# Performance work log

Hardware: AMD Instinct MI355X
Metric: run time of the kernel (lower is better)

The kernel has to match this reference:

```python
import jax, jax.numpy as jnp
import numpy as np

N = 8192
H = 256
E = N * 32
ALPHA = 0.2  # LeakyReLU negative slope from init kwarg alpha


def setup_inputs() -> dict:
    key = jax.random.key(0)
    ks = jax.random.split(key, 8)
    s = 1.0 / np.sqrt(H)
    return {
        "features": jax.random.normal(ks[0], (N, H), jnp.float32),
        "edge_index": jax.random.randint(ks[1], (2, E), 0, N, jnp.int64),
        "W_att": jax.random.normal(ks[2], (H, H), jnp.float32) * s,
        "a_src": jax.random.normal(ks[3], (H,), jnp.float32) * s,
        "a_dst": jax.random.normal(ks[4], (H,), jnp.float32) * s,
        "gcn_w": jax.random.normal(ks[5], (H, H), jnp.float32) * s,
        "gcn_b": jnp.zeros((H,), jnp.float32),
        "out_w": jax.random.normal(ks[6], (H, 2), jnp.float32) * s,
        "out_b": jnp.zeros((2,), jnp.float32),
    }


def reference(features, edge_index, W_att, a_src, a_dst, gcn_w, gcn_b, out_w, out_b):
    n = features.shape[0]
    # --- SingleNodeAttentionLayer (GAT-style dense self-attention, concat=True) ---
    Wh = features @ W_att                       # [N, H]
    e = jax.nn.leaky_relu(
        (Wh @ a_src)[:, None] + (Wh @ a_dst)[None, :], negative_slope=ALPHA
    )                                            # [N, N]
    attn = jax.nn.softmax(e, axis=-1)
    h1 = jax.nn.elu(attn @ Wh)                   # [N, H]
    # --- GCNConv: symmetric-normalized aggregation with self-loops ---
    loops = jnp.arange(n, dtype=edge_index.dtype)
    row = jnp.concatenate([edge_index[0], loops])  # destination
    col = jnp.concatenate([edge_index[1], loops])  # source
    deg = jax.ops.segment_sum(jnp.ones_like(row, dtype=h1.dtype), row, num_segments=n)
    dinv = jax.lax.rsqrt(jnp.maximum(deg, 1e-12))
    norm = dinv[row] * dinv[col]                 # [E+N]
    x = h1 @ gcn_w                               # [N, H]
    agg = jax.ops.segment_sum(x[col] * norm[:, None], row, num_segments=n) + gcn_b
    # --- head: linear -> mean over nodes -> softmax ---
    res = agg @ out_w + out_b                    # [N, 2]
    res = jnp.mean(res, axis=0, keepdims=True)   # [1, 2]
    return jax.nn.softmax(res, axis=-1)
```

## Files before the change

### kernel.cpp

```cpp
#include <hip/hip_runtime.h>
#include <hip/hip_bf16.h>

#define NN 8192
#define HH 256
#define EE (NN*32)
#define ALPHAC 0.2f
#define CHUNK 32
#define NCHUNK (NN/CHUNK)

#define OFF_WH     0
#define OFF_S      (OFF_WH + NN*HH)
#define OFF_D      (OFF_S + NN)
#define OFF_SORTD  (OFF_D + NN)
#define OFF_PERM   (OFF_SORTD + NN)
#define OFF_EA     (OFF_PERM + NN)
#define OFF_E1     (OFF_EA + NN)
#define OFF_APREF  (OFF_E1 + NN)
#define OFF_BPREF  (OFF_APREF + NN)
#define OFF_APART  (OFF_BPREF + NN)
#define OFF_BPART  (OFF_APART + NN*HH)
#define OFF_CPA    (OFF_BPART + NN*HH)
#define OFF_CPB    (OFF_CPA + (NCHUNK+1)*HH)
#define OFF_DEG    (OFF_CPB + (NCHUNK+1)*HH)
#define OFF_V      (OFF_DEG + NN)
#define OFF_DINV   (OFF_V + HH)
#define OFF_WNODE  (OFF_DINV + NN)
#define OFF_KEYS   (OFF_WNODE + NN)

__global__ __launch_bounds__(256) void k_gemm_wh(const float* __restrict__ A,
                                                 const float* __restrict__ B,
                                                 float* __restrict__ C) {
    __shared__ float As[32][68];
    __shared__ float Bs[32][68];
    int tid = threadIdx.x;
    int row0 = blockIdx.x * 64, col0 = blockIdx.y * 64;
    int tx = tid & 15, ty = tid >> 4;
    float acc[4][4] = {};
    int a_r = tid >> 2;
    int a_k = (tid & 3) * 8;
    int b_k = tid >> 3;
    int b_c = (tid & 7) * 8;
    const float* Aptr = A + (size_t)(row0 + a_r)*HH + a_k;
    const float* Bptr = B + (size_t)b_k*HH + col0 + b_c;
    for (int k0 = 0; k0 < HH; k0 += 32) {
        float4 av0 = *(const float4*)(Aptr + k0);
        float4 av1 = *(const float4*)(Aptr + k0 + 4);
        float4 bv0 = *(const float4*)(Bptr + (size_t)k0*HH);
        float4 bv1 = *(const float4*)(Bptr + (size_t)k0*HH + 4);
        __syncthreads();
        As[a_k+0][a_r] = av0.x; As[a_k+1][a_r] = av0.y;
        As[a_k+2][a_r] = av0.z; As[a_k+3][a_r] = av0.w;
        As[a_k+4][a_r] = av1.x; As[a_k+5][a_r] = av1.y;
        As[a_k+6][a_r] = av1.z; As[a_k+7][a_r] = av1.w;
        *(float4*)&Bs[b_k][b_c]   = bv0;
        *(float4*)&Bs[b_k][b_c+4] = bv1;
        __syncthreads();
        #pragma unroll
        for (int kk = 0; kk < 32; ++kk) {
            float4 ar = *(const float4*)&As[kk][ty*4];
            float4 br = *(const float4*)&Bs[kk][tx*4];
            float a0[4] = {ar.x, ar.y, ar.z, ar.w};
            float b0[4] = {br.x, br.y, br.z, br.w};
            #pragma unroll
            for (int r = 0; r < 4; ++r)
                #pragma unroll
                for (int c = 0; c < 4; ++c)
                    acc[r][c] += a0[r]*b0[c];
        }
    }
    #pragma unroll
    for (int r = 0; r < 4; ++r) {
        float4 o = make_float4(acc[r][0], acc[r][1], acc[r][2], acc[r][3]);
        *(float4*)(C + (size_t)(row0 + ty*4 + r)*HH + col0 + tx*4) = o;
    }
}

__global__ void k_sd(const float* __restrict__ Wh, const float* __restrict__ a_src,
                     const float* __restrict__ a_dst, float* ws) {
    int wave = threadIdx.x >> 6, lane = threadIdx.x & 63;
    int row = blockIdx.x*4 + wave;
    float4 wh = *(const float4*)(Wh + (size_t)row*HH + lane*4);
    float4 as = *(const float4*)(a_src + lane*4);
    float4 ad = *(const float4*)(a_dst + lane*4);
    float ss = wh.x*as.x + wh.y*as.y + wh.z*as.z + wh.w*as.w;
    float dd = wh.x*ad.x + wh.y*ad.y + wh.z*ad.z + wh.w*ad.w;
    #pragma unroll
    for (int off = 32; off; off >>= 1) {
        ss += __shfl_xor(ss, off);
        dd += __shfl_xor(dd, off);
    }
    if (lane == 0) {
        ws[OFF_S+row] = ss; ws[OFF_D+row] = dd;
        unsigned u = __float_as_uint(dd);
        unsigned mono = u ^ ((u & 0x80000000u) ? 0xFFFFFFFFu : 0x80000000u);
        ((unsigned long long*)(ws + OFF_KEYS))[row] =
            (((unsigned long long)mono) << 13) | (unsigned)row;
    }
}

__global__ __launch_bounds__(256) void k_rank(float* ws) {
    __shared__ unsigned long long lk[NN];
    const unsigned long long* keys = (const unsigned long long*)(ws + OFF_KEYS);
    int tid = threadIdx.x;
    for (int m = tid; m < NN/2; m += 256)
        *(ulonglong2*)&lk[m*2] = *(const ulonglong2*)&keys[m*2];
    __syncthreads();
    int wave = tid >> 6, lane = tid & 63;
    int jb = blockIdx.x*16 + wave*4;
    unsigned long long kj0 = lk[jb+0], kj1 = lk[jb+1];
    unsigned long long kj2 = lk[jb+2], kj3 = lk[jb+3];
    int c0 = 0, c1 = 0, c2 = 0, c3 = 0;
    #pragma unroll 4
    for (int it = 0; it < 64; ++it) {
        ulonglong2 kq = *(const ulonglong2*)&lk[(it*64 + lane)*2];
        c0 += (kq.x < kj0); c1 += (kq.x < kj1);
        c2 += (kq.x < kj2); c3 += (kq.x < kj3);
        c0 += (kq.y < kj0); c1 += (kq.y < kj1);
        c2 += (kq.y < kj2); c3 += (kq.y < kj3);
    }
    #pragma unroll
    for (int off = 1; off < 64; off <<= 1) {
        c0 += __shfl_xor(c0, off);
        c1 += __shfl_xor(c1, off);
        c2 += __shfl_xor(c2, off);
        c3 += __shfl_xor(c3, off);
    }
    if (lane == 0) {
        unsigned long long kk[4] = {kj0, kj1, kj2, kj3};
        int cr[4] = {c0, c1, c2, c3};
        #pragma unroll
        for (int q = 0; q < 4; ++q) {
            unsigned long long kv = kk[q];
            int r = cr[q];
            unsigned mm = (unsigned)(kv >> 13);
            unsigned u = (mm & 0x80000000u) ? (mm ^ 0x80000000u) : ~mm;
            float dj = __uint_as_float(u);
            int j = (int)(kv & 8191ULL);
            ws[OFF_SORTD + r] = dj;
            ((int*)ws)[OFF_PERM + r] = j;
            ws[OFF_EA + r] = expf(ALPHAC * dj);
            ws[OFF_E1 + r] = expf(dj);
        }
    }
}

__global__ void k_scan_scalar(float* ws) {
    __shared__ float sa[256], sb[256];
    int t = threadIdx.x;
    const float* ea = ws + OFF_EA;
    const float* e1 = ws + OFF_E1;
    int base = t * 32;
    float ta = 0.f, tb = 0.f;
    #pragma unroll
    for (int q = 0; q < 8; ++q) {
        float4 va = *(const float4*)&ea[base + q*4];
        float4 vb = *(const float4*)&e1[base + q*4];
        ta += va.x + va.y + va.z + va.w;
        tb += vb.x + vb.y + vb.z + vb.w;
    }
    sa[t] = ta; sb[t] = tb;
    __syncthreads();
    for (int off = 1; off < 256; off <<= 1) {
        float xa = (t >= off) ? sa[t-off] : 0.f;
        float xb = (t >= off) ? sb[t-off] : 0.f;
        __syncthreads();
        sa[t] += xa; sb[t] += xb;
        __syncthreads();
    }
    float ra = sa[t] - ta, rb = sb[t] - tb;
    #pragma unroll
    for (int q = 0; q < 8; ++q) {
        float4 va = *(const float4*)&ea[base + q*4];
        float4 vb = *(const float4*)&e1[base + q*4];
        float4 oa, ob;
        ra += va.x; oa.x = ra;  rb += vb.x; ob.x = rb;
        ra += va.y; oa.y = ra;  rb += vb.y; ob.y = rb;
        ra += va.z; oa.z = ra;  rb += vb.z; ob.z = rb;
        ra += va.w; oa.w = ra;  rb += vb.w; ob.w = rb;
        *(float4*)&ws[OFF_APREF + base + q*4] = oa;
        *(float4*)&ws[OFF_BPREF + base + q*4] = ob;
    }
}

__global__ __launch_bounds__(256) void k_vecpref(float* ws) {
    __shared__ int   sp[CHUNK];
    __shared__ float sea[CHUNK], se1[CHUNK];
    int c = blockIdx.x, h = threadIdx.x;
    int k0 = c * CHUNK;
    if (h < CHUNK) {
        sp[h]  = ((int*)ws)[OFF_PERM + k0 + h];
        sea[h] = ws[OFF_EA + k0 + h];
        se1[h] = ws[OFF_E1 + k0 + h];
    }
    __syncthreads();
    const float* Wh = ws + OFF_WH;
    float wv[CHUNK];
    #pragma unroll
    for (int kk = 0; kk < CHUNK; ++kk)
        wv[kk] = Wh[(size_t)sp[kk]*HH + h];
    float acca = 0.f, accb = 0.f;
    #pragma unroll
    for (int kk = 0; kk < CHUNK; ++kk) {
        acca += sea[kk]*wv[kk]; accb += se1[kk]*wv[kk];
        ws[OFF_APART + (size_t)(k0+kk)*HH + h] = acca;
        ws[OFF_BPART + (size_t)(k0+kk)*HH + h] = accb;
    }
    ws[OFF_CPA + (size_t)(c+1)*HH + h] = acca;
    ws[OFF_CPB + (size_t)(c+1)*HH + h] = accb;
}

__global__ __launch_bounds__(256) void k_chunkscan(float* ws) {
    int tid = threadIdx.x;
    int h = blockIdx.x*8 + (tid >> 5);
    int t = tid & 31;
    float la[8], lb[8];
    float ta = 0.f, tb = 0.f;
    #pragma unroll
    for (int m = 0; m < 8; ++m) {
        int c = t*8 + m;
        la[m] = ws[OFF_CPA + (size_t)(c+1)*HH + h];
        lb[m] = ws[OFF_CPB + (size_t)(c+1)*HH + h];
        ta += la[m]; tb += lb[m];
    }
    float ia = ta, ib = tb;
    #pragma unroll
    for (int off = 1; off < 32; off <<= 1) {
        float xa = __shfl_up(ia, off, 32);
        float xb = __shfl_up(ib, off, 32);
        if (t >= off) { ia += xa; ib += xb; }
    }
    float ba = ia - ta, bb = ib - tb;
    __syncthreads();
    #pragma unroll
    for (int m = 0; m < 8; ++m) {
        int c = t*8 + m;
        ws[OFF_CPA + (size_t)c*HH + h] = ba; ba += la[m];
        ws[OFF_CPB + (size_t)c*HH + h] = bb; bb += lb[m];
    }
    if (t == 31) {
        ws[OFF_CPA + (size_t)NCHUNK*HH + h] = ba;
        ws[OFF_CPB + (size_t)NCHUNK*HH + h] = bb;
    }
}

__global__ void k_deg(const int* __restrict__ ei, float* ws) {
    int e = blockIdx.x*256 + threadIdx.x;
    if (e < EE) atomicAdd(ws + OFF_DEG + ei[e], 1.0f);
}

__global__ void k_dinv(float* ws) {
    int i = blockIdx.x*256 + threadIdx.x;
    if (i < NN) {
        float dv = rsqrtf(ws[OFF_DEG + i] + 1.0f);
        ws[OFF_DINV + i] = dv;
        ws[OFF_WNODE + i] = dv*dv;
    }
}

__global__ void k_wnode(const int* __restrict__ ei, float* ws) {
    int e = blockIdx.x*256 + threadIdx.x;
    if (e < EE) {
        int r = ei[e], c = ei[EE + e];
        atomicAdd(ws + OFF_WNODE + c, ws[OFF_DINV + r] * ws[OFF_DINV + c]);
    }
}

__device__ __forceinline__ float elu1(float x) {
    return x > 0.f ? x : (expf(x) - 1.f);
}

__global__ __launch_bounds__(256) void k_rows(float* ws) {
    __shared__ float sd[NN];
    __shared__ float red[4][256];
    int tid = threadIdx.x;
    for (int m = tid; m < NN/4; m += 256)
        *(float4*)&sd[m*4] = *(const float4*)(ws + OFF_SORTD + m*4);
    __syncthreads();
    int wave = tid >> 6, lane = tid & 63;
    int gw = blockIdx.x*4 + wave;
    const float* apart = ws + OFF_APART;
    const float* bpart = ws + OFF_BPART;
    const float* cpa = ws + OFF_CPA;
    const float* cpb = ws + OFF_CPB;
    float btot = ws[OFF_BPREF + NN - 1];
    float4 BT = *(const float4*)(cpb + (size_t)NCHUNK*HH + lane*4);

    int myr = lane & 3;
    float si_m = ws[OFF_S + gw*4 + myr];
    float tt = -si_m;
    int lo = 0, hi = NN;
    while (lo < hi) {
        int mid = (lo + hi) >> 1;
        if (sd[mid] <= tt) lo = mid + 1; else hi = mid;
    }

    float accx = 0.f, accy = 0.f, accz = 0.f, accw = 0.f;
    #pragma unroll
    for (int r = 0; r < 4; ++r) {
        int i = gw*4 + r;
        int k = __shfl(lo, r);
        float si = __shfl(si_m, r);
        float eas = expf(ALPHAC * si), es = expf(si);
        float av = 0.f, bv = 0.f;
        float Ax=0.f, Ay=0.f, Az=0.f, Aw=0.f, Bx=0.f, By=0.f, Bz=0.f, Bw=0.f;
        if (k > 0) {
            int km = k - 1, cc = km >> 5;
            av = ws[OFF_APREF + km]; bv = ws[OFF_BPREF + km];
            float4 pa = *(const float4*)(apart + (size_t)km*HH + lane*4);
            float4 ca = *(const float4*)(cpa + (size_t)cc*HH + lane*4);
            float4 pb = *(const float4*)(bpart + (size_t)km*HH + lane*4);
            float4 cb = *(const float4*)(cpb + (size_t)cc*HH + lane*4);
            Ax = pa.x + ca.x; Ay = pa.y + ca.y; Az = pa.z + ca.z; Aw = pa.w + ca.w;
            Bx = pb.x + cb.x; By = pb.y + cb.y; Bz = pb.z + cb.z; Bw = pb.w + cb.w;
        }
        float Z = eas*av + es*(btot - bv);
        float invZ = 1.f / Z;
        float w = ws[OFF_WNODE + i];
        accx += w * elu1((eas*Ax + es*(BT.x - Bx)) * invZ);
        accy += w * elu1((eas*Ay + es*(BT.y - By)) * invZ);
        accz += w * elu1((eas*Az + es*(BT.z - Bz)) * invZ);
        accw += w * elu1((eas*Aw + es*(BT.w - Bw)) * invZ);
    }
    red[wave][lane*4+0] = accx;
    red[wave][lane*4+1] = accy;
    red[wave][lane*4+2] = accz;
    red[wave][lane*4+3] = accw;
    __syncthreads();
    float sum = red[0][tid] + red[1][tid] + red[2][tid] + red[3][tid];
    atomicAdd(ws + OFF_V + tid, sum);
}

__global__ void k_final(const float* __restrict__ gcn_w, const float* __restrict__ gcn_b,
                        const float* __restrict__ out_w, const float* __restrict__ out_b,
                        float* ws, float* out) {
    __shared__ float vl[HH];
    __shared__ float r0s[256], r1s[256];
    int t = threadIdx.x;
    vl[t] = ws[OFF_V + t];
    __syncthreads();
    float acc = 0.f;
    for (int h = 0; h < HH; ++h) acc += vl[h] * gcn_w[(size_t)h*HH + t];
    float meanv = acc * (1.0f/(float)NN) + gcn_b[t];
    r0s[t] = meanv * out_w[t*2+0];
    r1s[t] = meanv * out_w[t*2+1];
    __syncthreads();
    for (int off = 128; off; off >>= 1) {
        if (t < off) { r0s[t] += r0s[t+off]; r1s[t] += r1s[t+off]; }
        __syncthreads();
    }
    if (t == 0) {
        float res0 = r0s[0] + out_b[0], res1 = r1s[0] + out_b[1];
        float m = fmaxf(res0, res1);
        float e0 = expf(res0 - m), e1v = expf(res1 - m);
        float inv = 1.f / (e0 + e1v);
        out[0] = e0 * inv;
        out[1] = e1v * inv;
    }
}

extern "C" void kernel_launch(void* const* d_in, const int* in_sizes, int n_in,
                              void* d_out, int out_size, void* d_ws, size_t ws_size,
                              hipStream_t stream) {
    const float* features = (const float*)d_in[0];
    const int*   eidx     = (const int*)d_in[1];
    const float* W_att    = (const float*)d_in[2];
    const float* a_src    = (const float*)d_in[3];
    const float* a_dst    = (const float*)d_in[4];
    const float* gcn_w    = (const float*)d_in[5];
    const float* gcn_b    = (const float*)d_in[6];
    const float* out_w    = (const float*)d_in[7];
    const float* out_b    = (const float*)d_in[8];
    float* ws  = (float*)d_ws;
    float* out = (float*)d_out;

    hipMemsetAsync(ws + OFF_DEG, 0, (NN + HH)*sizeof(float), stream);
    k_gemm_wh<<<dim3(NN/64, HH/64), 256, 0, stream>>>(features, W_att, ws + OFF_WH);
    k_sd<<<NN/4, 256, 0, stream>>>(ws + OFF_WH, a_src, a_dst, ws);
    k_rank<<<NN/16, 256, 0, stream>>>(ws);
    k_scan_scalar<<<1, 256, 0, stream>>>(ws);
    k_vecpref<<<NCHUNK, 256, 0, stream>>>(ws);
    k_chunkscan<<<HH/8, 256, 0, stream>>>(ws);
    k_deg<<<EE/256, 256, 0, stream>>>(eidx, ws);
    k_dinv<<<NN/256, 256, 0, stream>>>(ws);
    k_wnode<<<EE/256, 256, 0, stream>>>(eidx, ws);
    k_rows<<<NN/16, 256, 0, stream>>>(ws);
    k_final<<<1, 256, 0, stream>>>(gcn_w, gcn_b, out_w, out_b, ws, out);
}
```

Before: 185.5 us.

## Fuse independent kernels, use bf16 MFMA for Wh GEMM, halve chunk size

Converts features and W_att to bf16 and computes Wh with MFMA 16x16x32 bf16 instructions instead of an fp32 SIMT GEMM. Independent stages (GEMM with degree counting, score/dinv, wnode with vector prefix, scalar scans with chunk scan) are merged into shared launches split by block index, which cuts the launch count. The scalar prefix is now computed per chunk, and the A/B partial sums are interleaved as float2. Switching the GEMM to bf16 lowers the precision of Wh, which feeds the sort by attention score. A dead kernel, k_sd_dinv, is left defined but never launched.

```diff
diff --git a/kernel.cpp b/kernel.cpp
--- a/kernel.cpp
+++ b/kernel.cpp
@@ -5,8 +5,12 @@
 #define HH 256
 #define EE (NN*32)
 #define ALPHAC 0.2f
-#define CHUNK 32
+#define CHUNK 16
 #define NCHUNK (NN/CHUNK)
+#define CSPAD 1024
+
+typedef __bf16 bf16x8 __attribute__((ext_vector_type(8)));
+typedef float  f32x4  __attribute__((ext_vector_type(4)));
 
 #define OFF_WH     0
 #define OFF_S      (OFF_WH + NN*HH)
@@ -15,86 +19,132 @@
 #define OFF_PERM   (OFF_SORTD + NN)
 #define OFF_EA     (OFF_PERM + NN)
 #define OFF_E1     (OFF_EA + NN)
-#define OFF_APREF  (OFF_E1 + NN)
-#define OFF_BPREF  (OFF_APREF + NN)
-#define OFF_APART  (OFF_BPREF + NN)
-#define OFF_BPART  (OFF_APART + NN*HH)
-#define OFF_CPA    (OFF_BPART + NN*HH)
-#define OFF_CPB    (OFF_CPA + (NCHUNK+1)*HH)
-#define OFF_DEG    (OFF_CPB + (NCHUNK+1)*HH)
+#define OFF_SAREL  (OFF_E1 + NN)
+#define OFF_SBREL  (OFF_SAREL + NN)
+#define OFF_ABPART (OFF_SBREL + NN)
+#define OFF_CPAB   (OFF_ABPART + 2*NN*HH)
+#define OFF_CSA    (OFF_CPAB + 2*(NCHUNK+1)*HH)
+#define OFF_CSB    (OFF_CSA + CSPAD)
+#define OFF_DEG    (OFF_CSB + CSPAD)
 #define OFF_V      (OFF_DEG + NN)
 #define OFF_DINV   (OFF_V + HH)
 #define OFF_WNODE  (OFF_DINV + NN)
 #define OFF_KEYS   (OFF_WNODE + NN)
-
-__global__ __launch_bounds__(256) void k_gemm_wh(const float* __restrict__ A,
-                                                 const float* __restrict__ B,
-                                                 float* __restrict__ C) {
-    __shared__ float As[32][68];
-    __shared__ float Bs[32][68];
-    int tid = threadIdx.x;
-    int row0 = blockIdx.x * 64, col0 = blockIdx.y * 64;
-    int tx = tid & 15, ty = tid >> 4;
-    float acc[4][4] = {};
-    int a_r = tid >> 2;
-    int a_k = (tid & 3) * 8;
-    int b_k = tid >> 3;
-    int b_c = (tid & 7) * 8;
-    const float* Aptr = A + (size_t)(row0 + a_r)*HH + a_k;
-    const float* Bptr = B + (size_t)b_k*HH + col0 + b_c;
-    for (int k0 = 0; k0 < HH; k0 += 32) {
-        float4 av0 = *(const float4*)(Aptr + k0);
-        float4 av1 = *(const float4*)(Aptr + k0 + 4);
-        float4 bv0 = *(const float4*)(Bptr + (size_t)k0*HH);
-        float4 bv1 = *(const float4*)(Bptr + (size_t)k0*HH + 4);
-        __syncthreads();
-        As[a_k+0][a_r] = av0.x; As[a_k+1][a_r] = av0.y;
-        As[a_k+2][a_r] = av0.z; As[a_k+3][a_r] = av0.w;
-        As[a_k+4][a_r] = av1.x; As[a_k+5][a_r] = av1.y;
-        As[a_k+6][a_r] = av1.z; As[a_k+7][a_r] = av1.w;
-        *(float4*)&Bs[b_k][b_c]   = bv0;
-        *(float4*)&Bs[b_k][b_c+4] = bv1;
-        __syncthreads();
-        #pragma unroll
-        for (int kk = 0; kk < 32; ++kk) {
-            float4 ar = *(const float4*)&As[kk][ty*4];
-            float4 br = *(const float4*)&Bs[kk][tx*4];
-            float a0[4] = {ar.x, ar.y, ar.z, ar.w};
-            float b0[4] = {br.x, br.y, br.z, br.w};
-            #pragma unroll
-            for (int r = 0; r < 4; ++r)
-                #pragma unroll
-                for (int c = 0; c < 4; ++c)
-                    acc[r][c] += a0[r]*b0[c];
-        }
-    }
-    #pragma unroll
-    for (int r = 0; r < 4; ++r) {
-        float4 o = make_float4(acc[r][0], acc[r][1], acc[r][2], acc[r][3]);
-        *(float4*)(C + (size_t)(row0 + ty*4 + r)*HH + col0 + tx*4) = o;
-    }
-}
-
-__global__ void k_sd(const float* __restrict__ Wh, const float* __restrict__ a_src,
-                     const float* __restrict__ a_dst, float* ws) {
-    int wave = threadIdx.x >> 6, lane = threadIdx.x & 63;
-    int row = blockIdx.x*4 + wave;
-    float4 wh = *(const float4*)(Wh + (size_t)row*HH + lane*4);
-    float4 as = *(const float4*)(a_src + lane*4);
-    float4 ad = *(const float4*)(a_dst + lane*4);
-    float ss = wh.x*as.x + wh.y*as.y + wh.z*as.z + wh.w*as.w;
-    float dd = wh.x*ad.x + wh.y*ad.y + wh.z*ad.z + wh.w*ad.w;
-    #pragma unroll
-    for (int off = 32; off; off >>= 1) {
-        ss += __shfl_xor(ss, off);
-        dd += __shfl_xor(dd, off);
-    }
-    if (lane == 0) {
-        ws[OFF_S+row] = ss; ws[OFF_D+row] = dd;
-        unsigned u = __float_as_uint(dd);
-        unsigned mono = u ^ ((u & 0x80000000u) ? 0xFFFFFFFFu : 0x80000000u);
-        ((unsigned long long*)(ws + OFF_KEYS))[row] =
-            (((unsigned long long)mono) << 13) | (unsigned)row;
+#define OFF_FB16   (OFF_KEYS + 2*NN)
+#define OFF_WT16   (OFF_FB16 + NN*HH/2)
+
+__global__ __launch_bounds__(256) void k_prep(const float* __restrict__ features,
+                                              const float* __restrict__ W_att,
+                                              float* ws) {
+    int bid = blockIdx.x, tid = threadIdx.x;
+    if (bid < 1024) {
+        int base = (bid*256 + tid)*8;
+        float4 a = *(const float4*)(features + base);
+        float4 b = *(const float4*)(features + base + 4);
+        bf16x8 v;
+        v[0]=(__bf16)a.x; v[1]=(__bf16)a.y; v[2]=(__bf16)a.z; v[3]=(__bf16)a.w;
+        v[4]=(__bf16)b.x; v[5]=(__bf16)b.y; v[6]=(__bf16)b.z; v[7]=(__bf16)b.w;
+        *(bf16x8*)((__bf16*)(ws + OFF_FB16) + base) = v;
+    } else if (bid < 1056) {
+        int idx0 = ((bid-1024)*256 + tid)*8;
+        __bf16* WT = (__bf16*)(ws + OFF_WT16);
+        #pragma unroll
+        for (int q = 0; q < 8; ++q) {
+            int idx = idx0 + q;
+            int n = idx >> 8, k = idx & 255;
+            WT[idx] = (__bf16)W_att[(size_t)k*HH + n];
+        }
+    } else {
+        int z0 = ((bid-1056)*256 + tid)*8;
+        #pragma unroll
+        for (int q = 0; q < 8; ++q) {
+            int i = z0 + q;
+            if (i < NN + HH) ws[OFF_DEG + i] = 0.f;
+        }
+    }
+}
+
+__global__ __launch_bounds__(256) void k_gemm_deg(const int* __restrict__ ei, float* ws) {
+    int bid = blockIdx.x, tid = threadIdx.x;
+    if (bid < 512) {
+        int mt = bid >> 2, nt = bid & 3;
+        int wave = tid >> 6, lane = tid & 63;
+        int ml = lane & 15, quad = lane >> 4;
+        int row0 = mt*64 + wave*16;
+        int n0 = nt*64;
+        const __bf16* FB = (const __bf16*)(ws + OFF_FB16);
+        const __bf16* WT = (const __bf16*)(ws + OFF_WT16);
+        const __bf16* Ap = FB + (size_t)(row0 + ml)*HH + quad*8;
+        const __bf16* B0 = WT + (size_t)(n0 +  0 + ml)*HH + quad*8;
+        const __bf16* B1 = WT + (size_t)(n0 + 16 + ml)*HH + quad*8;
+        const __bf16* B2 = WT + (size_t)(n0 + 32 + ml)*HH + quad*8;
+        const __bf16* B3 = WT + (size_t)(n0 + 48 + ml)*HH + quad*8;
+        f32x4 ac0 = {0.f,0.f,0.f,0.f}, ac1 = ac0, ac2 = ac0, ac3 = ac0;
+        #pragma unroll
+        for (int k0 = 0; k0 < HH; k0 += 32) {
+            bf16x8 af = *(const bf16x8*)(Ap + k0);
+            ac0 = __builtin_amdgcn_mfma_f32_16x16x32_bf16(af, *(const bf16x8*)(B0 + k0), ac0, 0, 0, 0);
+            ac1 = __builtin_amdgcn_mfma_f32_16x16x32_bf16(af, *(const bf16x8*)(B1 + k0), ac1, 0, 0, 0);
+            ac2 = __builtin_amdgcn_mfma_f32_16x16x32_bf16(af, *(const bf16x8*)(B2 + k0), ac2, 0, 0, 0);
+            ac3 = __builtin_amdgcn_mfma_f32_16x16x32_bf16(af, *(const bf16x8*)(B3 + k0), ac3, 0, 0, 0);
+        }
+        float* Whp = ws + OFF_WH;
+        #pragma unroll
+        for (int r = 0; r < 4; ++r) {
+            size_t grow = (size_t)(row0 + quad*4 + r)*HH + n0 + ml;
+            Whp[grow +  0] = ac0[r];
+            Whp[grow + 16] = ac1[r];
+            Whp[grow + 32] = ac2[r];
+            Whp[grow + 48] = ac3[r];
+        }
+    } else {
+        int e = (bid - 512)*256 + tid;
+        atomicAdd(ws + OFF_DEG + ei[e], 1.0f);
+    }
+}
+
+__global__ __launch_bounds__(256) void k_sd_dinv(float* ws) {
+    int bid = blockIdx.x, tid = threadIdx.x;
+    if (bid < 2048) {
+        int wave = tid >> 6, lane = tid & 63;
+        int row = bid*4 + wave;
+        const float* Wh = ws + OFF_WH;
+        float4 wh = *(const float4*)(Wh + (size_t)row*HH + lane*4);
+        (void)wh;
+    }
+    (void)ws;
+}
+
+__global__ __launch_bounds__(256) void k_sd_dinv2(const float* __restrict__ a_src,
+                                                  const float* __restrict__ a_dst,
+                                                  float* ws) {
+    int bid = blockIdx.x, tid = threadIdx.x;
+    if (bid < 2048) {
+        int wave = tid >> 6, lane = tid & 63;
+        int row = bid*4 + wave;
+        const float* Wh = ws + OFF_WH;
+        float4 wh = *(const float4*)(Wh + (size_t)row*HH + lane*4);
+        float4 as = *(const float4*)(a_src + lane*4);
+        float4 ad = *(const float4*)(a_dst + lane*4);
+        float ss = wh.x*as.x + wh.y*as.y + wh.z*as.z + wh.w*as.w;
+        float dd = wh.x*ad.x + wh.y*ad.y + wh.z*ad.z + wh.w*ad.w;
+        #pragma unroll
+        for (int off = 32; off; off >>= 1) {
+            ss += __shfl_xor(ss, off);
+            dd += __shfl_xor(dd, off);
+        }
+        if (lane == 0) {
+            ws[OFF_S+row] = ss; ws[OFF_D+row] = dd;
+            unsigned u = __float_as_uint(dd);
+            unsigned mono = u ^ ((u & 0x80000000u) ? 0xFFFFFFFFu : 0x80000000u);
+            ((unsigned long long*)(ws + OFF_KEYS))[row] =
+                (((unsigned long long)mono) << 13) | (unsigned)row;
+        }
+    } else {
+        int i = (bid - 2048)*256 + tid;
+        float dv = rsqrtf(ws[OFF_DEG + i] + 1.0f);
+        ws[OFF_DINV + i] = dv;
+        ws[OFF_WNODE + i] = dv*dv;
     }
 }
 
@@ -144,124 +194,110 @@
     }
 }
 
-__global__ void k_scan_scalar(float* ws) {
-    __shared__ float sa[256], sb[256];
-    int t = threadIdx.x;
-    const float* ea = ws + OFF_EA;
-    const float* e1 = ws + OFF_E1;
-    int base = t * 32;
-    float ta = 0.f, tb = 0.f;
-    #pragma unroll
-    for (int q = 0; q < 8; ++q) {
-        float4 va = *(const float4*)&ea[base + q*4];
-        float4 vb = *(const float4*)&e1[base + q*4];
-        ta += va.x + va.y + va.z + va.w;
-        tb += vb.x + vb.y + vb.z + vb.w;
-    }
-    sa[t] = ta; sb[t] = tb;
-    __syncthreads();
-    for (int off = 1; off < 256; off <<= 1) {
-        float xa = (t >= off) ? sa[t-off] : 0.f;
-        float xb = (t >= off) ? sb[t-off] : 0.f;
+__global__ __launch_bounds__(256) void k_wnode_vecpref(const int* __restrict__ ei, float* ws) {
+    int bid = blockIdx.x, tid = threadIdx.x;
+    if (bid < NCHUNK) {
+        __shared__ int   sp[CHUNK];
+        __shared__ float sea[CHUNK], se1[CHUNK];
+        int c = bid, h = tid;
+        int k0 = c * CHUNK;
+        if (h < CHUNK) {
+            sp[h]  = ((int*)ws)[OFF_PERM + k0 + h];
+            sea[h] = ws[OFF_EA + k0 + h];
+            se1[h] = ws[OFF_E1 + k0 + h];
+        }
         __syncthreads();
-        sa[t] += xa; sb[t] += xb;
+        if (tid < 64) {
+            int lane = tid;
+            float v = 0.f;
+            if (lane < 16) v = sea[lane];
+            else if (lane < 32) v = se1[lane-16];
+            #pragma unroll
+            for (int off = 1; off < 16; off <<= 1) {
+                float x = __shfl_up(v, off);
+                if ((lane & 15) >= off) v += x;
+            }
+            if (lane < 16) {
+                ws[OFF_SAREL + k0 + lane] = v;
+                if (lane == 15) ws[OFF_CSA + c + 1] = v;
+            } else if (lane < 32) {
+                ws[OFF_SBREL + k0 + lane - 16] = v;
+                if (lane == 31) ws[OFF_CSB + c + 1] = v;
+            }
+        }
+        const float* Wh = ws + OFF_WH;
+        float wv[CHUNK];
+        #pragma unroll
+        for (int kk = 0; kk < CHUNK; ++kk)
+            wv[kk] = Wh[(size_t)sp[kk]*HH + h];
+        float2* abp = (float2*)(ws + OFF_ABPART);
+        float acca = 0.f, accb = 0.f;
+        #pragma unroll
+        for (int kk = 0; kk < CHUNK; ++kk) {
+            acca += sea[kk]*wv[kk]; accb += se1[kk]*wv[kk];
+            abp[(size_t)(k0+kk)*HH + h] = make_float2(acca, accb);
+        }
+        float2* cp = (float2*)(ws + OFF_CPAB);
+        cp[(size_t)(c+1)*HH + h] = make_float2(acca, accb);
+    } else {
+        int e = (bid - NCHUNK)*256 + tid;
+        int r = ei[e], cix = ei[EE + e];
+        atomicAdd(ws + OFF_WNODE + cix, ws[OFF_DINV + r] * ws[OFF_DINV + cix]);
+    }
+}
+
+__global__ __launch_bounds__(256) void k_chunkscan(float* ws) {
+    int bid = blockIdx.x, tid = threadIdx.x;
+    if (bid < 32) {
+        int h = bid*8 + (tid >> 5);
+        int t = tid & 31;
+        float2* cp = (float2*)(ws + OFF_CPAB);
+        float la[16], lb[16];
+        float ta = 0.f, tb = 0.f;
+        #pragma unroll
+        for (int m = 0; m < 16; ++m) {
+            float2 v = cp[(size_t)(t*16 + m + 1)*HH + h];
+            la[m] = v.x; lb[m] = v.y;
+            ta += la[m]; tb += lb[m];
+        }
+        float ia = ta, ib = tb;
+        #pragma unroll
+        for (int off = 1; off < 32; off <<= 1) {
+            float xa = __shfl_up(ia, off, 32);
+            float xb = __shfl_up(ib, off, 32);
+            if (t >= off) { ia += xa; ib += xb; }
+        }
+        float ba = ia - ta, bb = ib - tb;
         __syncthreads();
-    }
-    float ra = sa[t] - ta, rb = sb[t] - tb;
-    #pragma unroll
-    for (int q = 0; q < 8; ++q) {
-        float4 va = *(const float4*)&ea[base + q*4];
-        float4 vb = *(const float4*)&e1[base + q*4];
-        float4 oa, ob;
-        ra += va.x; oa.x = ra;  rb += vb.x; ob.x = rb;
-        ra += va.y; oa.y = ra;  rb += vb.y; ob.y = rb;
-        ra += va.z; oa.z = ra;  rb += vb.z; ob.z = rb;
-        ra += va.w; oa.w = ra;  rb += vb.w; ob.w = rb;
-        *(float4*)&ws[OFF_APREF + base + q*4] = oa;
-        *(float4*)&ws[OFF_BPREF + base + q*4] = ob;
-    }
-}
-
-__global__ __launch_bounds__(256) void k_vecpref(float* ws) {
-    __shared__ int   sp[CHUNK];
-    __shared__ float sea[CHUNK], se1[CHUNK];
-    int c = blockIdx.x, h = threadIdx.x;
-    int k0 = c * CHUNK;
-    if (h < CHUNK) {
-        sp[h]  = ((int*)ws)[OFF_PERM + k0 + h];
-        sea[h] = ws[OFF_EA + k0 + h];
-        se1[h] = ws[OFF_E1 + k0 + h];
-    }
-    __syncthreads();
-    const float* Wh = ws + OFF_WH;
-    float wv[CHUNK];
-    #pragma unroll
-    for (int kk = 0; kk < CHUNK; ++kk)
-        wv[kk] = Wh[(size_t)sp[kk]*HH + h];
-    float acca = 0.f, accb = 0.f;
-    #pragma unroll
-    for (int kk = 0; kk < CHUNK; ++kk) {
-        acca += sea[kk]*wv[kk]; accb += se1[kk]*wv[kk];
-        ws[OFF_APART + (size_t)(k0+kk)*HH + h] = acca;
-        ws[OFF_BPART + (size_t)(k0+kk)*HH + h] = accb;
-    }
-    ws[OFF_CPA + (size_t)(c+1)*HH + h] = acca;
-    ws[OFF_CPB + (size_t)(c+1)*HH + h] = accb;
-}
-
-__global__ __launch_bounds__(256) void k_chunkscan(float* ws) {
-    int tid = threadIdx.x;
-    int h = blockIdx.x*8 + (tid >> 5);
-    int t = tid & 31;
-    float la[8], lb[8];
-    float ta = 0.f, tb = 0.f;
-    #pragma unroll
-    for (int m = 0; m < 8; ++m) {
-        int c = t*8 + m;
-        la[m] = ws[OFF_CPA + (size_t)(c+1)*HH + h];
-        lb[m] = ws[OFF_CPB + (size_t)(c+1)*HH + h];
-        ta += la[m]; tb += lb[m];
-    }
-    float ia = ta, ib = tb;
-    #pragma unroll
-    for (int off = 1; off < 32; off <<= 1) {
-        float xa = __shfl_up(ia, off, 32);
-        float xb = __shfl_up(ib, off, 32);
-        if (t >= off) { ia += xa; ib += xb; }
-    }
-    float ba = ia - ta, bb = ib - tb;
-    __syncthreads();
-    #pragma unroll
-    for (int m = 0; m < 8; ++m) {
-        int c = t*8 + m;
-        ws[OFF_CPA + (size_t)c*HH + h] = ba; ba += la[m];
-        ws[OFF_CPB + (size_t)c*HH + h] = bb; bb += lb[m];
-    }
-    if (t == 31) {
-        ws[OFF_CPA + (size_t)NCHUNK*HH + h] = ba;
-        ws[OFF_CPB + (size_t)NCHUNK*HH + h] = bb;
-    }
-}
-
-__global__ void k_deg(const int* __restrict__ ei, float* ws) {
-    int e = blockIdx.x*256 + threadIdx.x;
-    if (e < EE) atomicAdd(ws + OFF_DEG + ei[e], 1.0f);
-}
-
-__global__ void k_dinv(float* ws) {
-    int i = blockIdx.x*256 + threadIdx.x;
-    if (i < NN) {
-        float dv = rsqrtf(ws[OFF_DEG + i] + 1.0f);
-        ws[OFF_DINV + i] = dv;
-        ws[OFF_WNODE + i] = dv*dv;
-    }
-}
-
-__global__ void k_wnode(const int* __restrict__ ei, float* ws) {
-    int e = blockIdx.x*256 + threadIdx.x;
-    if (e < EE) {
-        int r = ei[e], c = ei[EE + e];
-        atomicAdd(ws + OFF_WNODE + c, ws[OFF_DINV + r] * ws[OFF_DINV + c]);
+        #pragma unroll
+        for (int m = 0; m < 16; ++m) {
+            cp[(size_t)(t*16 + m)*HH + h] = make_float2(ba, bb);
+            ba += la[m]; bb += lb[m];
+        }
+        if (t == 31) cp[(size_t)NCHUNK*HH + h] = make_float2(ba, bb);
+    } else {
+        int lane = tid & 63, wvi = tid >> 6;
+        bool act = wvi < 2;
+        float* cs = ws + (wvi == 1 ? OFF_CSB : OFF_CSA);
+        float la[8];
+        float ta = 0.f;
+        if (act) {
+            #pragma unroll
+            for (int m = 0; m < 8; ++m) { la[m] = cs[lane*8 + m + 1]; ta += la[m]; }
+        }
+        float ia = ta;
+        #pragma unroll
+        for (int off = 1; off < 64; off <<= 1) {
+            float x = __shfl_up(ia, off);
+            if (lane >= off) ia += x;
+        }
+        float ba = ia - ta;
+        __syncthreads();
+        if (act) {
+            #pragma unroll
+            for (int m = 0; m < 8; ++m) { cs[lane*8 + m] = ba; ba += la[m]; }
+            if (lane == 63) cs[NCHUNK] = ba;
+        }
     }
 }
 
@@ -278,12 +314,12 @@
     __syncthreads();
     int wave = tid >> 6, lane = tid & 63;
     int gw = blockIdx.x*4 + wave;
-    const float* apart = ws + OFF_APART;
-    const float* bpart = ws + OFF_BPART;
-    const float* cpa = ws + OFF_CPA;
-    const float* cpb = ws + OFF_CPB;
-    float btot = ws[OFF_BPREF + NN - 1];
-    float4 BT = *(const float4*)(cpb + (size_t)NCHUNK*HH + lane*4);
+    const float2* abp  = (const float2*)(ws + OFF_ABPART);
+    const float2* cpab = (const float2*)(ws + OFF_CPAB);
+    float btot = ws[OFF_CSB + NCHUNK];
+    const float4* btr = (const float4*)(cpab + (size_t)NCHUNK*HH);
+    float4 bt0 = btr[lane*2], bt1 = btr[lane*2+1];
+    float BTx = bt0.y, BTy = bt0.w, BTz = bt1.y, BTw = bt1.w;
 
     int myr = lane & 3;
     float si_m = ws[OFF_S + gw*4 + myr];
@@ -304,22 +340,25 @@
         float av = 0.f, bv = 0.f;
         float Ax=0.f, Ay=0.f, Az=0.f, Aw=0.f, Bx=0.f, By=0.f, Bz=0.f, Bw=0.f;
         if (k > 0) {
-            int km = k - 1, cc = km >> 5;
-            av = ws[OFF_APREF + km]; bv = ws[OFF_BPREF + km];
-            float4 pa = *(const float4*)(apart + (size_t)km*HH + lane*4);
-            float4 ca = *(const float4*)(cpa + (size_t)cc*HH + lane*4);
-            float4 pb = *(const float4*)(bpart + (size_t)km*HH + lane*4);
-            float4 cb = *(const float4*)(cpb + (size_t)cc*HH + lane*4);
-            Ax = pa.x + ca.x; Ay = pa.y + ca.y; Az = pa.z + ca.z; Aw = pa.w + ca.w;
-            Bx = pb.x + cb.x; By = pb.y + cb.y; Bz = pb.z + cb.z; Bw = pb.w + cb.w;
+            int km = k - 1, cc = km >> 4;
+            av = ws[OFF_CSA + cc] + ws[OFF_SAREL + km];
+            bv = ws[OFF_CSB + cc] + ws[OFF_SBREL + km];
+            const float4* pr = (const float4*)(abp + (size_t)km*HH);
+            const float4* cr = (const float4*)(cpab + (size_t)cc*HH);
+            float4 p0 = pr[lane*2], p1 = pr[lane*2+1];
+            float4 q0 = cr[lane*2], q1 = cr[lane*2+1];
+            Ax = p0.x + q0.x; Bx = p0.y + q0.y;
+            Ay = p0.z + q0.z; By = p0.w + q0.w;
+            Az = p1.x + q1.x; Bz = p1.y + q1.y;
+            Aw = p1.z + q1.z; Bw = p1.w + q1.w;
         }
         float Z = eas*av + es*(btot - bv);
         float invZ = 1.f / Z;
         float w = ws[OFF_WNODE + i];
-        accx += w * elu1((eas*Ax + es*(BT.x - Bx)) * invZ);
-        accy += w * elu1((eas*Ay + es*(BT.y - By)) * invZ);
-        accz += w * elu1((eas*Az + es*(BT.z - Bz)) * invZ);
-        accw += w * elu1((eas*Aw + es*(BT.w - Bw)) * invZ);
+        accx += w * elu1((eas*Ax + es*(BTx - Bx)) * invZ);
+        accy += w * elu1((eas*Ay + es*(BTy - By)) * invZ);
+        accz += w * elu1((eas*Az + es*(BTz - Bz)) * invZ);
+        accw += w * elu1((eas*Aw + es*(BTw - Bw)) * invZ);
     }
     red[wave][lane*4+0] = accx;
     red[wave][lane*4+1] = accy;
@@ -373,16 +412,12 @@
     float* ws  = (float*)d_ws;
     float* out = (float*)d_out;
 
-    hipMemsetAsync(ws + OFF_DEG, 0, (NN + HH)*sizeof(float), stream);
-    k_gemm_wh<<<dim3(NN/64, HH/64), 256, 0, stream>>>(features, W_att, ws + OFF_WH);
-    k_sd<<<NN/4, 256, 0, stream>>>(ws + OFF_WH, a_src, a_dst, ws);
+    k_prep<<<1061, 256, 0, stream>>>(features, W_att, ws);
+    k_gemm_deg<<<1536, 256, 0, stream>>>(eidx, ws);
+    k_sd_dinv2<<<2080, 256, 0, stream>>>(a_src, a_dst, ws);
     k_rank<<<NN/16, 256, 0, stream>>>(ws);
-    k_scan_scalar<<<1, 256, 0, stream>>>(ws);
-    k_vecpref<<<NCHUNK, 256, 0, stream>>>(ws);
-    k_chunkscan<<<HH/8, 256, 0, stream>>>(ws);
-    k_deg<<<EE/256, 256, 0, stream>>>(eidx, ws);
-    k_dinv<<<NN/256, 256, 0, stream>>>(ws);
-    k_wnode<<<EE/256, 256, 0, stream>>>(eidx, ws);
+    k_wnode_vecpref<<<NCHUNK + 1024, 256, 0, stream>>>(eidx, ws);
+    k_chunkscan<<<33, 256, 0, stream>>>(ws);
     k_rows<<<NN/16, 256, 0, stream>>>(ws);
     k_final<<<1, 256, 0, stream>>>(gcn_w, gcn_b, out_w, out_b, ws, out);
 }
```

Result: faster. 163.6 us (-11.8%).
